# Performance work log

Hardware: AMD Instinct MI355X
Metric: run time of the kernel (lower is better)

## Reference

```python
import jax, jax.numpy as jnp
import numpy as np

T = 8388608  # number of timesteps

def setup_inputs() -> dict:
    key = jax.random.key(0)
    x = jax.random.normal(key, (T,), dtype=jnp.float32)
    return {
        "x": x,
        "x0": jnp.float32(0.0),   # initial state estimate
        "p0": jnp.float32(1.0),   # initial covariance
        "A": jnp.float32(0.98),   # state transition
        "H": jnp.float32(1.0),    # observation model
        "Q": jnp.float32(0.01),   # process noise
        "R": jnp.float32(0.1),    # observation noise
    }

def reference(x, x0, p0, A, H, Q, R):
    # Scalar Kalman filter recurrence over T timesteps, expressed as lax.scan.
    def step(carry, y):
        xs, ps = carry
        x_pred = A * xs
        P_pred = A * ps * A + Q
        K = P_pred * H / (H * P_pred * H + R)
        x_new = x_pred + K * (y - H * x_pred)
        p_new = P_pred - K * H * P_pred
        return (x_new, p_new), x_new

    _, esti = jax.lax.scan(step, (x0, p0), x)
    return esti.reshape(x.shape[0], 1)  # matches torch reshape(len_sample, -1)
```

## Files before the change

kernel.cpp:

```cpp
#include <hip/hip_runtime.h>


#define T_TOTAL 8388608
#define PER_WAVE 1024
#define WARM 64
#define NWAVES (T_TOTAL / PER_WAVE)
#define NBLOCKS (NWAVES / 4)
#define CONV_ITERS 40
#define PRE 128

__global__ __launch_bounds__(256) void kalman_kernel(
    const float* __restrict__ x,
    const float* __restrict__ x0p, const float* __restrict__ p0p,
    const float* __restrict__ Aip, const float* __restrict__ Hip,
    const float* __restrict__ Qip, const float* __restrict__ Rip,
    float* __restrict__ out)
{
  const int lane = threadIdx.x & 63;
  const int wid  = (blockIdx.x << 2) | (threadIdx.x >> 6);
  const long base = (long)wid * PER_WAVE;

  float ys[16];
  {
    const float* xp = x + base + (lane << 4);
    *(float4*)(ys + 0)  = *(const float4*)(xp + 0);
    *(float4*)(ys + 4)  = *(const float4*)(xp + 4);
    *(float4*)(ys + 8)  = *(const float4*)(xp + 8);
    *(float4*)(ys + 12) = *(const float4*)(xp + 12);
  }
  float yw = 0.0f;
  if (wid > 0) yw = x[base - WARM + lane];

  const float A = Aip[0], H = Hip[0], Q = Qip[0], R = Rip[0];

  float p = p0p[0];
  #pragma unroll 4
  for (int i = 0; i < CONV_ITERS; ++i) {
    float Pp = A * p * A + Q;
    float K  = Pp * H / (H * Pp * H + R);
    p = Pp - K * H * Pp;
  }
  const float PpI  = A * p * A + Q;
  const float kInf = PpI * H / (H * PpI * H + R);
  const float aInf = A * (1.0f - kInf * H);

  __shared__ float sA[PRE], sK[PRE];
  if (blockIdx.x == 0) {
    if (threadIdx.x < PRE) {
      float pp = p0p[0];
      for (int i = 0; i < (int)threadIdx.x; ++i) {
        float Pp = A * pp * A + Q;
        float K  = Pp * H / (H * Pp * H + R);
        pp = Pp - K * H * Pp;
      }
      float Pp = A * pp * A + Q;
      float K  = Pp * H / (H * Pp * H + R);
      sA[threadIdx.x] = A * (1.0f - K * H);
      sK[threadIdx.x] = K;
    }
    __syncthreads();
  }

  float carry;
  if (wid == 0) {
    carry = x0p[0];
  } else {
    float As = aInf, Bs = kInf * yw;
    #pragma unroll
    for (int off = 1; off < 64; off <<= 1) {
      float Au = __shfl_up(As, off);
      float Bu = __shfl_up(Bs, off);
      if (lane >= off) { Bs = As * Bu + Bs; As = As * Au; }
    }
    carry = __shfl(Bs, 63);
  }

  auto run = [&](auto coef) {
    float Ac = 1.0f, Bc = 0.0f;
    #pragma unroll
    for (int j = 0; j < 16; ++j) {
      float a, k; coef(j, a, k);
      Bc = a * Bc + k * ys[j];
      Ac = a * Ac;
    }
    float As = Ac, Bs = Bc;
    #pragma unroll
    for (int off = 1; off < 64; off <<= 1) {
      float Au = __shfl_up(As, off);
      float Bu = __shfl_up(Bs, off);
      if (lane >= off) { Bs = As * Bu + Bs; As = As * Au; }
    }
    const float Axp = __shfl_up(As, 1);
    const float Bxp = __shfl_up(Bs, 1);
    float r = (lane == 0) ? carry : (Axp * carry + Bxp);
    #pragma unroll
    for (int j = 0; j < 16; ++j) {
      float a, k; coef(j, a, k);
      r = a * r + k * ys[j];
      ys[j] = r;
    }
    float* op = out + base + (lane << 4);
    *(float4*)(op + 0)  = *(const float4*)(ys + 0);
    *(float4*)(op + 4)  = *(const float4*)(ys + 4);
    *(float4*)(op + 8)  = *(const float4*)(ys + 8);
    *(float4*)(op + 12) = *(const float4*)(ys + 12);
  };

  if (wid == 0) {
    run([&](int j, float& a, float& k) {
      int e = (lane << 4) + j;
      if (e < PRE) { a = sA[e]; k = sK[e]; }
      else         { a = aInf;  k = kInf;  }
    });
  } else {
    run([&](int j, float& a, float& k) { a = aInf; k = kInf; });
  }
}

extern "C" void kernel_launch(void* const* d_in, const int* in_sizes, int n_in,
                              void* d_out, int out_size, void* d_ws, size_t ws_size,
                              hipStream_t stream) {
  const float* x  = (const float*)d_in[0];
  const float* x0 = (const float*)d_in[1];
  const float* p0 = (const float*)d_in[2];
  const float* A  = (const float*)d_in[3];
  const float* H  = (const float*)d_in[4];
  const float* Q  = (const float*)d_in[5];
  const float* R  = (const float*)d_in[6];
  float* out = (float*)d_out;

  kalman_kernel<<<NBLOCKS, 256, 0, stream>>>(x, x0, p0, A, H, Q, R, out);
}
```

Baseline: 99.10 us.

## Compute steady-state Kalman gain in closed form and use nontemporal stores

Replaces the iterative Riccati convergence loop and the block-0 shared-memory precompute of early gains with a closed-form solution of the scalar Riccati equation. The time-varying gain for the first wave comes from a Möbius-transform formula using exp2/log2, and the steady-state gain from the positive fixed point. Output stores become nontemporal. This removes per-thread serial divide chains and the shared-memory setup, at the cost of possible floating-point differences against the iterated recurrence.

```diff
diff --git a/kernel.cpp b/kernel.cpp
--- a/kernel.cpp
+++ b/kernel.cpp
@@ -6,8 +6,8 @@
 #define WARM 64
 #define NWAVES (T_TOTAL / PER_WAVE)
 #define NBLOCKS (NWAVES / 4)
-#define CONV_ITERS 40
-#define PRE 128
+
+typedef float f32x4 __attribute__((ext_vector_type(4)));
 
 __global__ __launch_bounds__(256) void kalman_kernel(
     const float* __restrict__ x,
@@ -23,43 +23,30 @@
   float ys[16];
   {
     const float* xp = x + base + (lane << 4);
-    *(float4*)(ys + 0)  = *(const float4*)(xp + 0);
-    *(float4*)(ys + 4)  = *(const float4*)(xp + 4);
-    *(float4*)(ys + 8)  = *(const float4*)(xp + 8);
-    *(float4*)(ys + 12) = *(const float4*)(xp + 12);
+    *(f32x4*)(ys + 0)  = *(const f32x4*)(xp + 0);
+    *(f32x4*)(ys + 4)  = *(const f32x4*)(xp + 4);
+    *(f32x4*)(ys + 8)  = *(const f32x4*)(xp + 8);
+    *(f32x4*)(ys + 12) = *(const f32x4*)(xp + 12);
   }
   float yw = 0.0f;
   if (wid > 0) yw = x[base - WARM + lane];
 
   const float A = Aip[0], H = Hip[0], Q = Qip[0], R = Rip[0];
+  const float p0 = p0p[0];
 
-  float p = p0p[0];
-  #pragma unroll 4
-  for (int i = 0; i < CONV_ITERS; ++i) {
-    float Pp = A * p * A + Q;
-    float K  = Pp * H / (H * Pp * H + R);
-    p = Pp - K * H * Pp;
-  }
-  const float PpI  = A * p * A + Q;
-  const float kInf = PpI * H / (H * PpI * H + R);
+  const float A2 = A * A, H2 = H * H;
+  const float bq   = R - A2 * R - Q * H2;
+  const float disc = sqrtf(bq * bq + 4.0f * H2 * Q * R);
+  const float f1 = ( disc - bq) / (2.0f * H2);
+  const float f2 = (-disc - bq) / (2.0f * H2);
+  const float kInf = f1 * H / (H2 * f1 + R);
   const float aInf = A * (1.0f - kInf * H);
-
-  __shared__ float sA[PRE], sK[PRE];
-  if (blockIdx.x == 0) {
-    if (threadIdx.x < PRE) {
-      float pp = p0p[0];
-      for (int i = 0; i < (int)threadIdx.x; ++i) {
-        float Pp = A * pp * A + Q;
-        float K  = Pp * H / (H * Pp * H + R);
-        pp = Pp - K * H * Pp;
-      }
-      float Pp = A * pp * A + Q;
-      float K  = Pp * H / (H * Pp * H + R);
-      sA[threadIdx.x] = A * (1.0f - K * H);
-      sK[threadIdx.x] = K;
-    }
-    __syncthreads();
-  }
+  const float tr  = A2 * R + Q * H2 + R;
+  const float s   = sqrtf(fmaxf(tr * tr - 4.0f * A2 * R * R, 0.0f));
+  const float rho = (tr - s) / (tr + s);
+  const float Pp0 = A2 * p0 + Q;
+  const float w0  = (Pp0 - f1) / (Pp0 - f2);
+  const float l2r = log2f(rho);
 
   float carry;
   if (wid == 0) {
@@ -100,17 +87,19 @@
       ys[j] = r;
     }
     float* op = out + base + (lane << 4);
-    *(float4*)(op + 0)  = *(const float4*)(ys + 0);
-    *(float4*)(op + 4)  = *(const float4*)(ys + 4);
-    *(float4*)(op + 8)  = *(const float4*)(ys + 8);
-    *(float4*)(op + 12) = *(const float4*)(ys + 12);
+    __builtin_nontemporal_store(*(const f32x4*)(ys + 0),  (f32x4*)(op + 0));
+    __builtin_nontemporal_store(*(const f32x4*)(ys + 4),  (f32x4*)(op + 4));
+    __builtin_nontemporal_store(*(const f32x4*)(ys + 8),  (f32x4*)(op + 8));
+    __builtin_nontemporal_store(*(const f32x4*)(ys + 12), (f32x4*)(op + 12));
   };
 
   if (wid == 0) {
     run([&](int j, float& a, float& k) {
-      int e = (lane << 4) + j;
-      if (e < PRE) { a = sA[e]; k = sK[e]; }
-      else         { a = aInf;  k = kInf;  }
+      float e  = (float)((lane << 4) + j);
+      float w  = w0 * exp2f(e * l2r);
+      float Pp = (f1 - f2 * w) / (1.0f - w);
+      k = Pp * H / (H2 * Pp + R);
+      a = A * (1.0f - k * H);
     });
   } else {
     run([&](int j, float& a, float& k) { a = aInf; k = kInf; });
```

Measured after the change: 106.7 us. 7.6% more time.
